# Optimization experiments

Hardware: AMD Instinct MI355X
Metric: run time of the kernel (lower is better)

Reference implementation:

```python
import jax, jax.numpy as jnp
import numpy as np
import math

B, L, H, P = 16, 2048, 512, 64


def setup_inputs() -> dict:
    key = jax.random.key(0)
    ks = jax.random.split(key, 10)
    s = 0.02
    return {
        "query": jax.random.normal(ks[0], (B, L, H), dtype=jnp.float32),
        "attention_mask": jax.random.randint(ks[1], (B, L), 0, 2, dtype=jnp.int32),
        "Wq": jax.random.normal(ks[2], (H, P), dtype=jnp.float32) * s,
        "bq": jnp.zeros((P,), dtype=jnp.float32),
        "Wk": jax.random.normal(ks[3], (H, P), dtype=jnp.float32) * s,
        "bk": jnp.zeros((P,), dtype=jnp.float32),
        "Wv": jax.random.normal(ks[4], (H, P), dtype=jnp.float32) * s,
        "bv": jnp.zeros((P,), dtype=jnp.float32),
        "Wo": jax.random.normal(ks[5], (P, H), dtype=jnp.float32) * s,
        "bo": jnp.zeros((H,), dtype=jnp.float32),
    }


def reference(query, attention_mask, Wq, bq, Wk, bk, Wv, bv, Wo, bo):
    # Linear projections (weights stored [in, out], equivalent to torch Linear)
    q = query @ Wq + bq  # [B, L, P]
    k = query @ Wk + bk  # [B, L, P]
    v = query @ Wv + bv  # [B, L, P]
    proj_dim = q.shape[-1]
    scores = jnp.einsum("bqp,bkp->bqk", q, k) / math.sqrt(proj_dim)  # [B, L, L]
    # Faithful to source: mask broadcasts over the LAST dim -> masks query rows
    mask = attention_mask.astype(scores.dtype)  # [B, L]
    scores = scores + (1.0 - mask[:, :, None]) * -10000.0
    attn = jax.nn.softmax(scores, axis=-1)  # [B, L, L]
    weighted = jnp.einsum("bqk,bkp->bqp", attn, v)  # [B, L, P]
    out = weighted @ Wo + bo  # [B, L, H]
    return out
```

## Files before the change

### kernel.cpp

```cpp
#include <hip/hip_runtime.h>

#define B_ 16
#define L_ 2048
#define H_ 512
#define P_ 64

typedef __attribute__((ext_vector_type(4))) float f32x4;
typedef __attribute__((ext_vector_type(8))) short short8;
typedef __attribute__((ext_vector_type(4))) short short4v;
typedef __attribute__((ext_vector_type(8))) __bf16 bf16x8;

#define DEVI static __device__ __forceinline__

#define QSCALE 0.18033688011112042f
#define MBIAS 16.0f

DEVI unsigned short f2bf(float f) {
  union { float f; unsigned u; } x; x.f = f;
  unsigned r = x.u + 0x7FFFu + ((x.u >> 16) & 1u);
  return (unsigned short)(r >> 16);
}

DEVI f32x4 mfma16(short8 a, short8 b, f32x4 c) {
  return __builtin_amdgcn_mfma_f32_16x16x32_bf16(
      __builtin_bit_cast(bf16x8, a), __builtin_bit_cast(bf16x8, b), c, 0, 0, 0);
}

DEVI short4v ld4s(const unsigned short* p) {
  return *reinterpret_cast<const short4v*>(p);
}

DEVI short8 pack8(short4v a, short4v b) {
  short8 r;
  r[0] = a[0]; r[1] = a[1]; r[2] = a[2]; r[3] = a[3];
  r[4] = b[0]; r[5] = b[1]; r[6] = b[2]; r[7] = b[3];
  return r;
}

DEVI void gll16(const void* src, void* ldsbase) {
  __builtin_amdgcn_global_load_lds(
      (const __attribute__((address_space(1))) void*)src,
      (__attribute__((address_space(3))) void*)ldsbase, 16, 0, 0);
}

__global__ __launch_bounds__(256) void k_prep(
    const float* __restrict__ Wq, const float* __restrict__ Wk,
    const float* __restrict__ Wv, const float* __restrict__ Wo,
    unsigned short* __restrict__ WtG, unsigned short* __restrict__ WoT)
{
  __shared__ unsigned short TS[64][72];
  const int tid = threadIdx.x;
  const int m = blockIdx.x >> 3;
  const int tile = blockIdx.x & 7;
  const int rr = tid >> 2;
  const int c0 = (tid & 3) * 16;
  const float* src = (m == 0) ? Wq : (m == 1) ? Wk : (m == 2) ? Wv : Wo;

  const float* sp = (m < 3) ? src + (long)(tile * 64 + rr) * 64 + c0
                            : src + (long)rr * 512 + tile * 64 + c0;
#pragma unroll
  for (int j4 = 0; j4 < 4; ++j4) {
    float4 v = *reinterpret_cast<const float4*>(sp + 4 * j4);
    TS[rr][c0 + 4 * j4 + 0] = f2bf(v.x);
    TS[rr][c0 + 4 * j4 + 1] = f2bf(v.y);
    TS[rr][c0 + 4 * j4 + 2] = f2bf(v.z);
    TS[rr][c0 + 4 * j4 + 3] = f2bf(v.w);
  }
  __syncthreads();
  short8 v0, v1;
#pragma unroll
  for (int j = 0; j < 8; ++j) {
    v0[j] = (short)TS[c0 + j][rr];
    v1[j] = (short)TS[c0 + 8 + j][rr];
  }
  unsigned short* dp = (m < 3)
      ? WtG + m * 32768 + rr * 512 + tile * 64 + c0
      : WoT + (tile * 64 + rr) * 64 + c0;
  *reinterpret_cast<short8*>(dp) = v0;
  *reinterpret_cast<short8*>(dp + 8) = v1;
}

__global__ __launch_bounds__(256) void k_qkv(
    const float* __restrict__ query,
    const float* __restrict__ bq, const float* __restrict__ bk,
    const float* __restrict__ bv,
    const unsigned short* __restrict__ WtG,
    unsigned short* __restrict__ qbf, unsigned short* __restrict__ kbf,
    unsigned short* __restrict__ vT)
{
  __shared__ float At[2][64][32];
  __shared__ unsigned short Wt[2][192][32];
  __shared__ unsigned short VS[64][72];
  const int tid = threadIdx.x;
  const int lane = tid & 63;
  const int w = tid >> 6;
  const int g = lane >> 4;
  const int ln = lane & 15;
  const long row0 = (long)blockIdx.x * 64;
  const f32x4 fzero = {0.f, 0.f, 0.f, 0.f};

  const int srA = w * 16 + (lane >> 3);
  const int scA = (lane & 7) * 16;
  const int swsA = (srA & 7) << 4;
  const int srW = w * 48 + (lane >> 2);
  const int scW = (lane & 3) * 16;
  const int swsW = (srW & 3) << 4;
  const char* qbase = (const char*)(query + row0 * (long)H_);
  const char* wbase = (const char*)WtG;

  f32x4 acc[12];
#pragma unroll
  for (int t = 0; t < 12; ++t) acc[t] = fzero;

  auto stage = [&](int cc, int k0) {
    gll16(qbase + (long)srA * 2048 + k0 * 4 + (scA ^ swsA),
          (char*)&At[cc][0][0] + w * 2048);
    gll16(qbase + (long)(srA + 8) * 2048 + k0 * 4 + (scA ^ swsA),
          (char*)&At[cc][0][0] + w * 2048 + 1024);
#pragma unroll
    for (int jj = 0; jj < 3; ++jj) {
      int r = srW + 16 * jj;
      gll16(wbase + (long)r * 1024 + k0 * 2 + (scW ^ swsW),
            (char*)&Wt[cc][0][0] + w * 3072 + jj * 1024);
    }
  };

  stage(0, 0);
  __syncthreads();
  int cur = 0;
  const int swA = (ln & 7) << 4;
  const int swW = (ln & 3) << 4;
  for (int k0 = 0; k0 < H_; k0 += 32) {
    if (k0 + 32 < H_) stage(cur ^ 1, k0 + 32);
    const char* ar = (const char*)&At[cur][16 * w + ln][0];
    float4 a0 = *reinterpret_cast<const float4*>(ar + ((16 * g) ^ swA));
    float4 a1 = *reinterpret_cast<const float4*>(ar + ((64 + 16 * g) ^ swA));
    short8 af;
    af[0] = (short)f2bf(a0.x); af[1] = (short)f2bf(a0.y);
    af[2] = (short)f2bf(a0.z); af[3] = (short)f2bf(a0.w);
    af[4] = (short)f2bf(a1.x); af[5] = (short)f2bf(a1.y);
    af[6] = (short)f2bf(a1.z); af[7] = (short)f2bf(a1.w);
#pragma unroll
    for (int t = 0; t < 12; ++t) {
      const char* wr =
          (const char*)&Wt[cur][(t >> 2) * 64 + (t & 3) * 16 + ln][0];
      short8 bfr = pack8(
          *reinterpret_cast<const short4v*>(wr + ((8 * g) ^ swW)),
          *reinterpret_cast<const short4v*>(wr + ((32 + 8 * g) ^ swW)));
      acc[t] = mfma16(af, bfr, acc[t]);
    }
    __syncthreads();
    cur ^= 1;
  }

  const long rbase = row0 + 16 * w;
#pragma unroll
  for (int t = 0; t < 4; ++t) {
    float bb = bq[t * 16 + ln];
#pragma unroll
    for (int r = 0; r < 4; ++r)
      qbf[(rbase + 4 * g + r) * P_ + t * 16 + ln] =
          f2bf((acc[t][r] + bb) * QSCALE);
  }
#pragma unroll
  for (int t = 0; t < 4; ++t) {
    float bb = bk[t * 16 + ln];
#pragma unroll
    for (int r = 0; r < 4; ++r)
      kbf[(rbase + 4 * g + r) * P_ + t * 16 + ln] = f2bf(acc[4 + t][r] + bb);
  }
#pragma unroll
  for (int t = 0; t < 4; ++t) {
    float bb = bv[t * 16 + ln];
#pragma unroll
    for (int r = 0; r < 4; ++r)
      VS[t * 16 + ln][16 * w + 4 * g + r] = f2bf(acc[8 + t][r] + bb);
  }
  __syncthreads();
  {
    const int p = tid >> 2;
    const int c0 = (tid & 3) * 16;
    const long bb = row0 >> 11;
    const long rl = row0 & 2047;
    unsigned short* dst = vT + bb * (long)(P_ * L_) + (long)p * L_ + rl + c0;
    *reinterpret_cast<short8*>(dst) =
        *reinterpret_cast<const short8*>(&VS[p][c0]);
    *reinterpret_cast<short8*>(dst + 8) =
        *reinterpret_cast<const short8*>(&VS[p][c0 + 8]);
  }
}

__global__ __launch_bounds__(256) void k_attn(
    const unsigned short* __restrict__ qbf,
    const unsigned short* __restrict__ kbf,
    const unsigned short* __restrict__ vT,
    unsigned short* __restrict__ wbf)
{
  __shared__ unsigned short Kt[2][64][64];
  __shared__ unsigned short Vt[2][64][64];
  __shared__ unsigned short OT[64][72];
  const int tid = threadIdx.x;
  const int lane = tid & 63;
  const int wv = tid >> 6;
  const int g = lane >> 4;
  const int ln = lane & 15;
  const int bid = (blockIdx.x & 7) * 64 + (blockIdx.x >> 3);
  const int b = bid >> 5;
  const int qt = bid & 31;
  const unsigned short* qb = qbf + (long)b * (L_ * P_);
  const char* kbase = (const char*)(kbf + (long)b * (L_ * P_));
  const char* vbase = (const char*)(vT + (long)b * (P_ * L_));
  const f32x4 fzero = {0.f, 0.f, 0.f, 0.f};

  const int q = qt * 64 + 16 * wv + ln;
  const unsigned short* qp = qb + (long)q * P_;
  const short8 qf0 = pack8(ld4s(qp + 4 * g), ld4s(qp + 16 + 4 * g));
  const short8 qf1 = pack8(ld4s(qp + 32 + 4 * g), ld4s(qp + 48 + 4 * g));

  const int sr = wv * 16 + (lane >> 3);
  const int sc = (lane & 7) * 16;
  const int sws = (sr & 7) << 4;

  auto stageKV = [&](int cc, int kv0) {
    gll16(kbase + (long)(kv0 + sr) * 128 + (sc ^ sws),
          (char*)&Kt[cc][0][0] + wv * 2048);
    gll16(kbase + (long)(kv0 + sr + 8) * 128 + (sc ^ sws),
          (char*)&Kt[cc][0][0] + wv * 2048 + 1024);
    gll16(vbase + (long)sr * 4096 + kv0 * 2 + (sc ^ sws),
          (char*)&Vt[cc][0][0] + wv * 2048);
    gll16(vbase + (long)(sr + 8) * 4096 + kv0 * 2 + (sc ^ sws),
          (char*)&Vt[cc][0][0] + wv * 2048 + 1024);
  };

  f32x4 o[4];
#pragma unroll
  for (int t = 0; t < 4; ++t) o[t] = fzero;
  float lsum = 0.f;

  stageKV(0, 0);
  __syncthreads();
  int cur = 0;
  const int sw = (ln & 7) << 4;
  for (int kv0 = 0; kv0 < L_; kv0 += 64) {
    if (kv0 + 64 < L_) stageKV(cur ^ 1, kv0 + 64);
    f32x4 s[4];
#pragma unroll
    for (int t = 0; t < 4; ++t) {
      const char* kr = (const char*)&Kt[cur][16 * t + ln][0];
      short8 kf0 = pack8(
          *reinterpret_cast<const short4v*>(kr + ((8 * g) ^ sw)),
          *reinterpret_cast<const short4v*>(kr + ((32 + 8 * g) ^ sw)));
      short8 kf1 = pack8(
          *reinterpret_cast<const short4v*>(kr + ((64 + 8 * g) ^ sw)),
          *reinterpret_cast<const short4v*>(kr + ((96 + 8 * g) ^ sw)));
      s[t] = mfma16(kf0, qf0, fzero);
      s[t] = mfma16(kf1, qf1, s[t]);
    }
    float pp[4][4];
#pragma unroll
    for (int t = 0; t < 4; ++t)
#pragma unroll
      for (int r = 0; r < 4; ++r) {
        pp[t][r] = exp2f(s[t][r] - MBIAS);
        lsum += pp[t][r];
      }
    short8 pa0, pa1;
#pragma unroll
    for (int j = 0; j < 4; ++j) {
      pa0[j] = (short)f2bf(pp[0][j]);
      pa0[4 + j] = (short)f2bf(pp[1][j]);
      pa1[j] = (short)f2bf(pp[2][j]);
      pa1[4 + j] = (short)f2bf(pp[3][j]);
    }
#pragma unroll
    for (int t = 0; t < 4; ++t) {
      const char* vr = (const char*)&Vt[cur][16 * t + ln][0];
      short8 vf0 = pack8(
          *reinterpret_cast<const short4v*>(vr + ((8 * g) ^ sw)),
          *reinterpret_cast<const short4v*>(vr + ((32 + 8 * g) ^ sw)));
      short8 vf1 = pack8(
          *reinterpret_cast<const short4v*>(vr + ((64 + 8 * g) ^ sw)),
          *reinterpret_cast<const short4v*>(vr + ((96 + 8 * g) ^ sw)));
      o[t] = mfma16(vf0, pa0, o[t]);
      o[t] = mfma16(vf1, pa1, o[t]);
    }
    __syncthreads();
    cur ^= 1;
  }

  lsum += __shfl_xor(lsum, 16);
  lsum += __shfl_xor(lsum, 32);
  const float linv = 1.0f / lsum;

#pragma unroll
  for (int t = 0; t < 4; ++t)
#pragma unroll
    for (int r = 0; r < 4; ++r)
      OT[16 * wv + ln][16 * t + 4 * g + r] = f2bf(o[t][r] * linv);
  __syncthreads();
  {
    const int qr = tid >> 2;
    const int c0 = (tid & 3) * 16;
    unsigned short* dst = wbf + ((long)b * L_ + qt * 64 + qr) * P_ + c0;
    *reinterpret_cast<short8*>(dst) =
        *reinterpret_cast<const short8*>(&OT[qr][c0]);
    *reinterpret_cast<short8*>(dst + 8) =
        *reinterpret_cast<const short8*>(&OT[qr][c0 + 8]);
  }
}

__global__ __launch_bounds__(256) void k_out(
    const unsigned short* __restrict__ wbf,
    const unsigned short* __restrict__ WoT,
    const float* __restrict__ bo, float* __restrict__ out)
{
  const int tid = threadIdx.x;
  const int lane = tid & 63;
  const int w = tid >> 6;
  const int g = lane >> 4;
  const int ln = lane & 15;
  const long row0 = (long)blockIdx.x * 64;
  const f32x4 fzero = {0.f, 0.f, 0.f, 0.f};

  const unsigned short* ap = wbf + (row0 + 16 * w + ln) * P_;
  const short8 af0 = pack8(ld4s(ap + 4 * g), ld4s(ap + 16 + 4 * g));
  const short8 af1 = pack8(ld4s(ap + 32 + 4 * g), ld4s(ap + 48 + 4 * g));

  for (int t = 0; t < 32; ++t) {
    const int n = 16 * t + ln;
    const unsigned short* wp = WoT + n * 64;
    short8 b0 = pack8(ld4s(wp + 4 * g), ld4s(wp + 16 + 4 * g));
    short8 b1 = pack8(ld4s(wp + 32 + 4 * g), ld4s(wp + 48 + 4 * g));
    f32x4 acc = mfma16(af0, b0, fzero);
    acc = mfma16(af1, b1, acc);
    const float bb = bo[n];
#pragma unroll
    for (int r = 0; r < 4; ++r)
      out[(row0 + 16 * w + 4 * g + r) * (long)H_ + n] = acc[r] + bb;
  }
}

extern "C" void kernel_launch(void* const* d_in, const int* in_sizes, int n_in,
                              void* d_out, int out_size, void* d_ws, size_t ws_size,
                              hipStream_t stream)
{
  const float* query = (const float*)d_in[0];
  const float* Wq = (const float*)d_in[2];
  const float* bq = (const float*)d_in[3];
  const float* Wk = (const float*)d_in[4];
  const float* bk = (const float*)d_in[5];
  const float* Wv = (const float*)d_in[6];
  const float* bv = (const float*)d_in[7];
  const float* Wo = (const float*)d_in[8];
  const float* bo = (const float*)d_in[9];
  float* out = (float*)d_out;

  const long M = (long)B_ * L_;
  unsigned short* qbf = (unsigned short*)d_ws;
  unsigned short* kbf = qbf + M * P_;
  unsigned short* vTp = kbf + M * P_;
  unsigned short* wbf = vTp + M * P_;
  unsigned short* WtG = wbf + M * P_;
  unsigned short* WoT = WtG + 3 * 64 * 512;

  k_prep<<<dim3(32), dim3(256), 0, stream>>>(Wq, Wk, Wv, Wo, WtG, WoT);
  k_qkv<<<dim3(M / 64), dim3(256), 0, stream>>>(
      query, bq, bk, bv, WtG, qbf, kbf, vTp);
  k_attn<<<dim3(B_ * (L_ / 64)), dim3(256), 0, stream>>>(qbf, kbf, vTp, wbf);
  k_out<<<dim3(M / 64), dim3(256), 0, stream>>>(wbf, WoT, bo, out);
}
```

Measured before the change: 230.7 us.

## Rotate LDS swizzle for wide fragment reads, packed bf16 converts, stage Wo in LDS

```diff
diff --git a/kernel.cpp b/kernel.cpp
--- a/kernel.cpp
+++ b/kernel.cpp
@@ -6,6 +6,7 @@
 #define P_ 64
 
 typedef __attribute__((ext_vector_type(4))) float f32x4;
+typedef __attribute__((ext_vector_type(4))) unsigned int u32x4;
 typedef __attribute__((ext_vector_type(8))) short short8;
 typedef __attribute__((ext_vector_type(4))) short short4v;
 typedef __attribute__((ext_vector_type(8))) __bf16 bf16x8;
@@ -19,6 +20,12 @@
   union { float f; unsigned u; } x; x.f = f;
   unsigned r = x.u + 0x7FFFu + ((x.u >> 16) & 1u);
   return (unsigned short)(r >> 16);
+}
+
+DEVI unsigned cvtpk(float lo, float hi) {
+  unsigned d;
+  asm("v_cvt_pk_bf16_f32 %0, %1, %2" : "=v"(d) : "v"(lo), "v"(hi));
+  return d;
 }
 
 DEVI f32x4 mfma16(short8 a, short8 b, f32x4 c) {
@@ -88,9 +95,9 @@
     unsigned short* __restrict__ qbf, unsigned short* __restrict__ kbf,
     unsigned short* __restrict__ vT)
 {
-  __shared__ float At[2][64][32];
-  __shared__ unsigned short Wt[2][192][32];
-  __shared__ unsigned short VS[64][72];
+  extern __shared__ char smem[];
+  char* At = smem;
+  char* Wt = smem + 16384;
   const int tid = threadIdx.x;
   const int lane = tid & 63;
   const int w = tid >> 6;
@@ -100,11 +107,8 @@
   const f32x4 fzero = {0.f, 0.f, 0.f, 0.f};
 
   const int srA = w * 16 + (lane >> 3);
-  const int scA = (lane & 7) * 16;
-  const int swsA = (srA & 7) << 4;
-  const int srW = w * 48 + (lane >> 2);
-  const int scW = (lane & 3) * 16;
-  const int swsW = (srW & 3) << 4;
+  const int sgA = ((lane & 7) - (lane >> 3)) & 7;
+  const int sgW = ((lane & 3) - ((lane >> 2) & 3)) & 3;
   const char* qbase = (const char*)(query + row0 * (long)H_);
   const char* wbase = (const char*)WtG;
 
@@ -113,15 +117,15 @@
   for (int t = 0; t < 12; ++t) acc[t] = fzero;
 
   auto stage = [&](int cc, int k0) {
-    gll16(qbase + (long)srA * 2048 + k0 * 4 + (scA ^ swsA),
-          (char*)&At[cc][0][0] + w * 2048);
-    gll16(qbase + (long)(srA + 8) * 2048 + k0 * 4 + (scA ^ swsA),
-          (char*)&At[cc][0][0] + w * 2048 + 1024);
+    gll16(qbase + (long)srA * 2048 + k0 * 4 + sgA * 16,
+          At + cc * 8192 + w * 2048);
+    gll16(qbase + (long)(srA + 8) * 2048 + k0 * 4 + sgA * 16,
+          At + cc * 8192 + w * 2048 + 1024);
 #pragma unroll
     for (int jj = 0; jj < 3; ++jj) {
-      int r = srW + 16 * jj;
-      gll16(wbase + (long)r * 1024 + k0 * 2 + (scW ^ swsW),
-            (char*)&Wt[cc][0][0] + w * 3072 + jj * 1024);
+      int r = w * 48 + jj * 16 + (lane >> 2);
+      gll16(wbase + (long)r * 1024 + k0 * 2 + sgW * 16,
+            Wt + cc * 12288 + w * 3072 + jj * 1024);
     }
   };
 
@@ -132,21 +136,21 @@
   const int swW = (ln & 3) << 4;
   for (int k0 = 0; k0 < H_; k0 += 32) {
     if (k0 + 32 < H_) stage(cur ^ 1, k0 + 32);
-    const char* ar = (const char*)&At[cur][16 * w + ln][0];
-    float4 a0 = *reinterpret_cast<const float4*>(ar + ((16 * g) ^ swA));
-    float4 a1 = *reinterpret_cast<const float4*>(ar + ((64 + 16 * g) ^ swA));
-    short8 af;
-    af[0] = (short)f2bf(a0.x); af[1] = (short)f2bf(a0.y);
-    af[2] = (short)f2bf(a0.z); af[3] = (short)f2bf(a0.w);
-    af[4] = (short)f2bf(a1.x); af[5] = (short)f2bf(a1.y);
-    af[6] = (short)f2bf(a1.z); af[7] = (short)f2bf(a1.w);
+    const char* ar = At + cur * 8192 + (16 * w + ln) * 128;
+    float4 a_lo = *reinterpret_cast<const float4*>(ar + ((32 * g + swA) & 127));
+    float4 a_hi =
+        *reinterpret_cast<const float4*>(ar + ((32 * g + 16 + swA) & 127));
+    u32x4 aw;
+    aw[0] = cvtpk(a_lo.x, a_lo.y);
+    aw[1] = cvtpk(a_lo.z, a_lo.w);
+    aw[2] = cvtpk(a_hi.x, a_hi.y);
+    aw[3] = cvtpk(a_hi.z, a_hi.w);
+    short8 af = __builtin_bit_cast(short8, aw);
 #pragma unroll
     for (int t = 0; t < 12; ++t) {
-      const char* wr =
-          (const char*)&Wt[cur][(t >> 2) * 64 + (t & 3) * 16 + ln][0];
-      short8 bfr = pack8(
-          *reinterpret_cast<const short4v*>(wr + ((8 * g) ^ swW)),
-          *reinterpret_cast<const short4v*>(wr + ((32 + 8 * g) ^ swW)));
+      const char* wr = Wt + cur * 12288 + (t * 16 + ln) * 64;
+      short8 bfr =
+          *reinterpret_cast<const short8*>(wr + ((16 * g + swW) & 63));
       acc[t] = mfma16(af, bfr, acc[t]);
     }
     __syncthreads();
@@ -169,6 +173,7 @@
     for (int r = 0; r < 4; ++r)
       kbf[(rbase + 4 * g + r) * P_ + t * 16 + ln] = f2bf(acc[4 + t][r] + bb);
   }
+  unsigned short (*VS)[72] = (unsigned short(*)[72])smem;
 #pragma unroll
   for (int t = 0; t < 4; ++t) {
     float bb = bv[t * 16 + ln];
@@ -196,9 +201,9 @@
     const unsigned short* __restrict__ vT,
     unsigned short* __restrict__ wbf)
 {
-  __shared__ unsigned short Kt[2][64][64];
-  __shared__ unsigned short Vt[2][64][64];
-  __shared__ unsigned short OT[64][72];
+  extern __shared__ char smem[];
+  char* Kb = smem;
+  char* Vb = smem + 16384;
   const int tid = threadIdx.x;
   const int lane = tid & 63;
   const int wv = tid >> 6;
@@ -212,24 +217,22 @@
   const char* vbase = (const char*)(vT + (long)b * (P_ * L_));
   const f32x4 fzero = {0.f, 0.f, 0.f, 0.f};
 
-  const int q = qt * 64 + 16 * wv + ln;
-  const unsigned short* qp = qb + (long)q * P_;
-  const short8 qf0 = pack8(ld4s(qp + 4 * g), ld4s(qp + 16 + 4 * g));
-  const short8 qf1 = pack8(ld4s(qp + 32 + 4 * g), ld4s(qp + 48 + 4 * g));
-
-  const int sr = wv * 16 + (lane >> 3);
-  const int sc = (lane & 7) * 16;
-  const int sws = (sr & 7) << 4;
+  const unsigned short* qp = qb + (long)(qt * 64 + 16 * wv + ln) * P_;
+  const short8 qf0 = *reinterpret_cast<const short8*>(qp + 8 * g);
+  const short8 qf1 = *reinterpret_cast<const short8*>(qp + 32 + 8 * g);
+
+  const int srow = wv * 16 + (lane >> 3);
+  const int sg = ((lane & 7) - (lane >> 3)) & 7;
 
   auto stageKV = [&](int cc, int kv0) {
-    gll16(kbase + (long)(kv0 + sr) * 128 + (sc ^ sws),
-          (char*)&Kt[cc][0][0] + wv * 2048);
-    gll16(kbase + (long)(kv0 + sr + 8) * 128 + (sc ^ sws),
-          (char*)&Kt[cc][0][0] + wv * 2048 + 1024);
-    gll16(vbase + (long)sr * 4096 + kv0 * 2 + (sc ^ sws),
-          (char*)&Vt[cc][0][0] + wv * 2048);
-    gll16(vbase + (long)(sr + 8) * 4096 + kv0 * 2 + (sc ^ sws),
-          (char*)&Vt[cc][0][0] + wv * 2048 + 1024);
+    gll16(kbase + (long)(kv0 + srow) * 128 + sg * 16,
+          Kb + cc * 8192 + wv * 2048);
+    gll16(kbase + (long)(kv0 + srow + 8) * 128 + sg * 16,
+          Kb + cc * 8192 + wv * 2048 + 1024);
+    gll16(vbase + (long)srow * 4096 + kv0 * 2 + sg * 16,
+          Vb + cc * 8192 + wv * 2048);
+    gll16(vbase + (long)(srow + 8) * 4096 + kv0 * 2 + sg * 16,
+          Vb + cc * 8192 + wv * 2048 + 1024);
   };
 
   f32x4 o[4];
@@ -246,13 +249,11 @@
     f32x4 s[4];
 #pragma unroll
     for (int t = 0; t < 4; ++t) {
-      const char* kr = (const char*)&Kt[cur][16 * t + ln][0];
-      short8 kf0 = pack8(
-          *reinterpret_cast<const short4v*>(kr + ((8 * g) ^ sw)),
-          *reinterpret_cast<const short4v*>(kr + ((32 + 8 * g) ^ sw)));
-      short8 kf1 = pack8(
-          *reinterpret_cast<const short4v*>(kr + ((64 + 8 * g) ^ sw)),
-          *reinterpret_cast<const short4v*>(kr + ((96 + 8 * g) ^ sw)));
+      const char* kr = Kb + cur * 8192 + (16 * t + ln) * 128;
+      short8 kf0 =
+          *reinterpret_cast<const short8*>(kr + ((16 * g + sw) & 127));
+      short8 kf1 =
+          *reinterpret_cast<const short8*>(kr + ((64 + 16 * g + sw) & 127));
       s[t] = mfma16(kf0, qf0, fzero);
       s[t] = mfma16(kf1, qf1, s[t]);
     }
@@ -264,23 +265,22 @@
         pp[t][r] = exp2f(s[t][r] - MBIAS);
         lsum += pp[t][r];
       }
-    short8 pa0, pa1;
-#pragma unroll
-    for (int j = 0; j < 4; ++j) {
-      pa0[j] = (short)f2bf(pp[0][j]);
-      pa0[4 + j] = (short)f2bf(pp[1][j]);
-      pa1[j] = (short)f2bf(pp[2][j]);
-      pa1[4 + j] = (short)f2bf(pp[3][j]);
-    }
+    u32x4 w0, w1;
+    w0[0] = cvtpk(pp[0][0], pp[0][1]); w0[1] = cvtpk(pp[0][2], pp[0][3]);
+    w0[2] = cvtpk(pp[1][0], pp[1][1]); w0[3] = cvtpk(pp[1][2], pp[1][3]);
+    w1[0] = cvtpk(pp[2][0], pp[2][1]); w1[1] = cvtpk(pp[2][2], pp[2][3]);
+    w1[2] = cvtpk(pp[3][0], pp[3][1]); w1[3] = cvtpk(pp[3][2], pp[3][3]);
+    short8 pa0 = __builtin_bit_cast(short8, w0);
+    short8 pa1 = __builtin_bit_cast(short8, w1);
 #pragma unroll
     for (int t = 0; t < 4; ++t) {
-      const char* vr = (const char*)&Vt[cur][16 * t + ln][0];
+      const char* vr = Vb + cur * 8192 + (16 * t + ln) * 128;
       short8 vf0 = pack8(
-          *reinterpret_cast<const short4v*>(vr + ((8 * g) ^ sw)),
-          *reinterpret_cast<const short4v*>(vr + ((32 + 8 * g) ^ sw)));
+          *reinterpret_cast<const short4v*>(vr + ((8 * g + sw) & 127)),
+          *reinterpret_cast<const short4v*>(vr + ((32 + 8 * g + sw) & 127)));
       short8 vf1 = pack8(
-          *reinterpret_cast<const short4v*>(vr + ((64 + 8 * g) ^ sw)),
-          *reinterpret_cast<const short4v*>(vr + ((96 + 8 * g) ^ sw)));
+          *reinterpret_cast<const short4v*>(vr + ((64 + 8 * g + sw) & 127)),
+          *reinterpret_cast<const short4v*>(vr + ((96 + 8 * g + sw) & 127)));
       o[t] = mfma16(vf0, pa0, o[t]);
       o[t] = mfma16(vf1, pa1, o[t]);
     }
@@ -292,6 +292,7 @@
   lsum += __shfl_xor(lsum, 32);
   const float linv = 1.0f / lsum;
 
+  unsigned short (*OT)[72] = (unsigned short(*)[72])smem;
 #pragma unroll
   for (int t = 0; t < 4; ++t)
 #pragma unroll
@@ -314,6 +315,7 @@
     const unsigned short* __restrict__ WoT,
     const float* __restrict__ bo, float* __restrict__ out)
 {
+  __shared__ unsigned short WoL[512][64];
   const int tid = threadIdx.x;
   const int lane = tid & 63;
   const int w = tid >> 6;
@@ -321,16 +323,30 @@
   const int ln = lane & 15;
   const long row0 = (long)blockIdx.x * 64;
   const f32x4 fzero = {0.f, 0.f, 0.f, 0.f};
+  const char* wobase = (const char*)WoT;
+
+  {
+    const int sg = ((lane & 7) - (lane >> 3)) & 7;
+#pragma unroll
+    for (int jj = 0; jj < 16; ++jj) {
+      int r = w * 128 + jj * 8 + (lane >> 3);
+      gll16(wobase + (long)r * 128 + sg * 16,
+            (char*)&WoL[0][0] + w * 16384 + jj * 1024);
+    }
+  }
+  __syncthreads();
 
   const unsigned short* ap = wbf + (row0 + 16 * w + ln) * P_;
-  const short8 af0 = pack8(ld4s(ap + 4 * g), ld4s(ap + 16 + 4 * g));
-  const short8 af1 = pack8(ld4s(ap + 32 + 4 * g), ld4s(ap + 48 + 4 * g));
+  const short8 af0 = *reinterpret_cast<const short8*>(ap + 8 * g);
+  const short8 af1 = *reinterpret_cast<const short8*>(ap + 32 + 8 * g);
+  const int sw = (ln & 7) << 4;
 
   for (int t = 0; t < 32; ++t) {
     const int n = 16 * t + ln;
-    const unsigned short* wp = WoT + n * 64;
-    short8 b0 = pack8(ld4s(wp + 4 * g), ld4s(wp + 16 + 4 * g));
-    short8 b1 = pack8(ld4s(wp + 32 + 4 * g), ld4s(wp + 48 + 4 * g));
+    const char* wr = (const char*)&WoL[n][0];
+    short8 b0 = *reinterpret_cast<const short8*>(wr + ((16 * g + sw) & 127));
+    short8 b1 =
+        *reinterpret_cast<const short8*>(wr + ((64 + 16 * g + sw) & 127));
     f32x4 acc = mfma16(af0, b0, fzero);
     acc = mfma16(af1, b1, acc);
     const float bb = bo[n];
@@ -364,8 +380,9 @@
   unsigned short* WoT = WtG + 3 * 64 * 512;
 
   k_prep<<<dim3(32), dim3(256), 0, stream>>>(Wq, Wk, Wv, Wo, WtG, WoT);
-  k_qkv<<<dim3(M / 64), dim3(256), 0, stream>>>(
+  k_qkv<<<dim3(M / 64), dim3(256), 40960, stream>>>(
       query, bq, bk, bv, WtG, qbf, kbf, vTp);
-  k_attn<<<dim3(B_ * (L_ / 64)), dim3(256), 0, stream>>>(qbf, kbf, vTp, wbf);
+  k_attn<<<dim3(B_ * (L_ / 64)), dim3(256), 32768, stream>>>(
+      qbf, kbf, vTp, wbf);
   k_out<<<dim3(M / 64), dim3(256), 0, stream>>>(wbf, WoT, bo, out);
 }
```

Measured after the change: 189.1 us. 18.0% less time.
